# Kernel optimization log

Measured on AMD Instinct MI355X. Metric: run time of the kernel, lower is better.

Reference implementation:

```python
import jax, jax.numpy as jnp
import numpy as np

B, N, D, F = 32, 4096, 256, 256

def setup_inputs() -> dict:
    key = jax.random.key(0)
    k1, k2, k3, k4 = jax.random.split(key, 4)
    raw_input = jax.random.normal(k1, (B, N, D), dtype=jnp.float32)
    input_plus_attention = jax.random.normal(k2, (B, F), dtype=jnp.float32)
    W = jax.random.normal(k3, (F, N), dtype=jnp.float32) * 0.02
    b = jnp.zeros((N,), dtype=jnp.float32)
    # keras 'uniform' initializer: U(-0.05, 0.05)
    threshold = jax.random.uniform(k4, (1,), minval=-0.05, maxval=0.05, dtype=jnp.float32)
    return {"raw_input": raw_input, "input_plus_attention": input_plus_attention,
            "W": W, "b": b, "threshold": threshold}

def reference(raw_input, input_plus_attention, W, b, threshold):
    # Dense(units, relu): [B,F] @ [F,N] -> [B,N]
    x = jax.nn.relu(input_plus_attention @ W + b)
    # BinaryLayer: 1.0 where x > threshold else 0.0 -> row selection mask [B,N]
    mask = x > threshold[0]
    # TF boolean_mask + reshape(B,-1,D) performs per-batch stream compaction of
    # selected rows. JAX needs static shapes, so compact selected rows to the
    # front (stable order preserved) and zero-pad the tail to length N.
    order = jnp.argsort(jnp.where(mask, 0, 1).astype(jnp.int32), axis=1)  # stable: selected first
    gathered = jnp.take_along_axis(raw_input, order[:, :, None], axis=1)  # [B,N,D]
    counts = jnp.sum(mask, axis=1, keepdims=True)                          # [B,1]
    keep = jnp.arange(N)[None, :] < counts                                 # [B,N]
    out = jnp.where(keep[:, :, None], gathered, jnp.zeros((), raw_input.dtype))
    return out
```

## Files before the change

### kernel.cpp

```cpp
#include <hip/hip_runtime.h>
#include <hip/hip_bf16.h>
#include <stdint.h>


#define BB 32
#define NN 4096
#define DD 256
#define FF 256
#define ASTRIDE (FF + 4)
#define RPB 32

typedef float f4 __attribute__((ext_vector_type(4)));

__global__ __launch_bounds__(256) void mask_kernel(
    const float* __restrict__ A,
    const float* __restrict__ W,
    const float* __restrict__ bias,
    const float* __restrict__ thr_p,
    uint8_t* __restrict__ bits8)
{
    __shared__ float a_sh[BB * ASTRIDE];
    __shared__ float wT[8 * ASTRIDE];

    const int t     = threadIdx.x;
    const int chunk = blockIdx.x;
    const int n0    = chunk * 8;

    for (int i = t; i < BB * FF; i += 256) {
        int b = i >> 8, f = i & 255;
        a_sh[b * ASTRIDE + f] = A[i];
    }
    for (int i = t; i < FF * 8; i += 256) {
        int f = i >> 3, c = i & 7;
        wT[c * ASTRIDE + f] = W[(size_t)f * NN + n0 + c];
    }
    __syncthreads();

    const float thr = thr_p[0];
    const int c = t & 7;
    const int b = t >> 3;

    const f4* ap = reinterpret_cast<const f4*>(a_sh + b * ASTRIDE);
    const f4* wp = reinterpret_cast<const f4*>(wT   + c * ASTRIDE);

    double s0 = 0.0, s1 = 0.0, s2 = 0.0, s3 = 0.0;
    #pragma unroll 8
    for (int fs = 0; fs < FF / 4; ++fs) {
        f4 a4 = ap[fs];
        f4 w4 = wp[fs];
        s0 = fma((double)a4.x, (double)w4.x, s0);
        s1 = fma((double)a4.y, (double)w4.y, s1);
        s2 = fma((double)a4.z, (double)w4.z, s2);
        s3 = fma((double)a4.w, (double)w4.w, s3);
    }
    const float v = (float)((s0 + s1) + (s2 + s3)) + bias[n0 + c];
    const int m = (fmaxf(v, 0.f) > thr) ? 1 : 0;

    unsigned long long bal = __ballot(m);
    if (c == 0) {
        const int g = (t & 63) >> 3;
        bits8[b * 512 + chunk] = (uint8_t)((bal >> (8 * g)) & 0xFF);
    }
}

__global__ __launch_bounds__(256) void gather_kernel(
    const float* __restrict__ raw,
    const uint16_t* __restrict__ bits,
    float* __restrict__ out)
{
    const int b   = blockIdx.y;
    const int t   = threadIdx.x;
    const int j0b = blockIdx.x * RPB;

    __shared__ int wsum[4];
    __shared__ int cnt_sh;
    __shared__ int order_sh[RPB];

    unsigned m = bits[b * 256 + t];
    const int s = __popc(m);

    const int lane = t & 63;
    const int wid  = t >> 6;
    int incl = s;
    #pragma unroll
    for (int d = 1; d < 64; d <<= 1) {
        int x = __shfl_up(incl, d, 64);
        if (lane >= d) incl += x;
    }
    if (lane == 63) wsum[wid] = incl;
    __syncthreads();
    if (t == 0) {
        int run = 0;
        #pragma unroll
        for (int i = 0; i < 4; ++i) { int x = wsum[i]; wsum[i] = run; run += x; }
        cnt_sh = run;
    }
    __syncthreads();

    int base = wsum[wid] + (incl - s);
    if (base < j0b + RPB && base + s > j0b) {
        const int n0 = t * 16;
        while (m) {
            const int pos = __ffs(m) - 1;
            const unsigned rel = (unsigned)(base - j0b);
            if (rel < RPB) order_sh[rel] = n0 + pos;
            ++base;
            if (base >= j0b + RPB) break;
            m &= m - 1;
        }
    }
    __syncthreads();

    const int cnt = cnt_sh;
    const f4* rawb = reinterpret_cast<const f4*>(raw) + (size_t)b * NN * (DD / 4);
    f4*       outb = reinterpret_cast<f4*>(out)       + (size_t)b * NN * (DD / 4);
    const int j0 = j0b + wid * 8;

    #pragma unroll
    for (int g = 0; g < 2; ++g) {
        const int r = j0 + g * 4;
        const int rr = r - j0b;
        f4 v0 = {0.f, 0.f, 0.f, 0.f};
        f4 v1 = {0.f, 0.f, 0.f, 0.f};
        f4 v2 = {0.f, 0.f, 0.f, 0.f};
        f4 v3 = {0.f, 0.f, 0.f, 0.f};
        if (r + 0 < cnt) v0 = rawb[(size_t)order_sh[rr + 0] * (DD / 4) + lane];
        if (r + 1 < cnt) v1 = rawb[(size_t)order_sh[rr + 1] * (DD / 4) + lane];
        if (r + 2 < cnt) v2 = rawb[(size_t)order_sh[rr + 2] * (DD / 4) + lane];
        if (r + 3 < cnt) v3 = rawb[(size_t)order_sh[rr + 3] * (DD / 4) + lane];
        __builtin_nontemporal_store(v0, &outb[(size_t)(r + 0) * (DD / 4) + lane]);
        __builtin_nontemporal_store(v1, &outb[(size_t)(r + 1) * (DD / 4) + lane]);
        __builtin_nontemporal_store(v2, &outb[(size_t)(r + 2) * (DD / 4) + lane]);
        __builtin_nontemporal_store(v3, &outb[(size_t)(r + 3) * (DD / 4) + lane]);
    }
}

extern "C" void kernel_launch(void* const* d_in, const int* in_sizes, int n_in,
                              void* d_out, int out_size, void* d_ws, size_t ws_size,
                              hipStream_t stream) {
    const float* raw  = (const float*)d_in[0];
    const float* A    = (const float*)d_in[1];
    const float* W    = (const float*)d_in[2];
    const float* bias = (const float*)d_in[3];
    const float* thr  = (const float*)d_in[4];
    float* out = (float*)d_out;

    uint8_t* bits8 = (uint8_t*)d_ws;

    mask_kernel<<<512, 256, 0, stream>>>(A, W, bias, thr, bits8);
    gather_kernel<<<dim3(NN / RPB, BB), 256, 0, stream>>>(
        raw, (const uint16_t*)bits8, out);
}
```

Before: 55.85 us.

## Convert compaction gather into scatter with coalesced source loads and split zero-fill

Each block now loads its 32 contiguous source rows up front with non-temporal loads, overlapping them with the prefix scan. It computes destination indices per source row and scatters only the selected rows. Zero-padding of the tail is distributed evenly across blocks. This trades selective reads for full contiguous reads, increasing read traffic when few rows are selected, in exchange for early, coalesced loads and a simpler index build.

```diff
diff --git a/kernel.cpp b/kernel.cpp
--- a/kernel.cpp
+++ b/kernel.cpp
@@ -9,6 +9,7 @@
 #define FF 256
 #define ASTRIDE (FF + 4)
 #define RPB 32
+#define NBLK (NN / RPB)
 
 typedef float f4 __attribute__((ext_vector_type(4)));
 
@@ -68,19 +69,34 @@
     const uint16_t* __restrict__ bits,
     float* __restrict__ out)
 {
-    const int b   = blockIdx.y;
-    const int t   = threadIdx.x;
-    const int j0b = blockIdx.x * RPB;
+    const int b    = blockIdx.y;
+    const int bx   = blockIdx.x;
+    const int t    = threadIdx.x;
+    const int lane = t & 63;
+    const int wid  = t >> 6;
 
     __shared__ int wsum[4];
     __shared__ int cnt_sh;
-    __shared__ int order_sh[RPB];
+    __shared__ int dst_sh[RPB];
+
+    const f4* rawb = reinterpret_cast<const f4*>(raw) + (size_t)b * NN * (DD / 4);
+    f4*       outb = reinterpret_cast<f4*>(out)       + (size_t)b * NN * (DD / 4);
+    const int srow = bx * RPB + wid * 8;
+
+    f4 v0 = __builtin_nontemporal_load(&rawb[(size_t)(srow + 0) * (DD / 4) + lane]);
+    f4 v1 = __builtin_nontemporal_load(&rawb[(size_t)(srow + 1) * (DD / 4) + lane]);
+    f4 v2 = __builtin_nontemporal_load(&rawb[(size_t)(srow + 2) * (DD / 4) + lane]);
+    f4 v3 = __builtin_nontemporal_load(&rawb[(size_t)(srow + 3) * (DD / 4) + lane]);
+    f4 v4 = __builtin_nontemporal_load(&rawb[(size_t)(srow + 4) * (DD / 4) + lane]);
+    f4 v5 = __builtin_nontemporal_load(&rawb[(size_t)(srow + 5) * (DD / 4) + lane]);
+    f4 v6 = __builtin_nontemporal_load(&rawb[(size_t)(srow + 6) * (DD / 4) + lane]);
+    f4 v7 = __builtin_nontemporal_load(&rawb[(size_t)(srow + 7) * (DD / 4) + lane]);
+
+    if (t < RPB) dst_sh[t] = -1;
 
     unsigned m = bits[b * 256 + t];
     const int s = __popc(m);
 
-    const int lane = t & 63;
-    const int wid  = t >> 6;
     int incl = s;
     #pragma unroll
     for (int d = 1; d < 64; d <<= 1) {
@@ -97,42 +113,44 @@
     }
     __syncthreads();
 
-    int base = wsum[wid] + (incl - s);
-    if (base < j0b + RPB && base + s > j0b) {
-        const int n0 = t * 16;
-        while (m) {
-            const int pos = __ffs(m) - 1;
-            const unsigned rel = (unsigned)(base - j0b);
-            if (rel < RPB) order_sh[rel] = n0 + pos;
-            ++base;
-            if (base >= j0b + RPB) break;
-            m &= m - 1;
+    const int wchunk0 = bx * 2;
+    if (t == wchunk0 || t == wchunk0 + 1) {
+        const int loc0 = (t - wchunk0) * 16;
+        int d = wsum[wid] + (incl - s);
+        unsigned mm = m;
+        while (mm) {
+            const int pos = __ffs(mm) - 1;
+            dst_sh[loc0 + pos] = d++;
+            mm &= mm - 1;
         }
     }
     __syncthreads();
 
+    const int r0 = wid * 8;
+    const int d0 = dst_sh[r0 + 0];
+    const int d1 = dst_sh[r0 + 1];
+    const int d2 = dst_sh[r0 + 2];
+    const int d3 = dst_sh[r0 + 3];
+    const int d4 = dst_sh[r0 + 4];
+    const int d5 = dst_sh[r0 + 5];
+    const int d6 = dst_sh[r0 + 6];
+    const int d7 = dst_sh[r0 + 7];
+    if (d0 >= 0) __builtin_nontemporal_store(v0, &outb[(size_t)d0 * (DD / 4) + lane]);
+    if (d1 >= 0) __builtin_nontemporal_store(v1, &outb[(size_t)d1 * (DD / 4) + lane]);
+    if (d2 >= 0) __builtin_nontemporal_store(v2, &outb[(size_t)d2 * (DD / 4) + lane]);
+    if (d3 >= 0) __builtin_nontemporal_store(v3, &outb[(size_t)d3 * (DD / 4) + lane]);
+    if (d4 >= 0) __builtin_nontemporal_store(v4, &outb[(size_t)d4 * (DD / 4) + lane]);
+    if (d5 >= 0) __builtin_nontemporal_store(v5, &outb[(size_t)d5 * (DD / 4) + lane]);
+    if (d6 >= 0) __builtin_nontemporal_store(v6, &outb[(size_t)d6 * (DD / 4) + lane]);
+    if (d7 >= 0) __builtin_nontemporal_store(v7, &outb[(size_t)d7 * (DD / 4) + lane]);
+
     const int cnt = cnt_sh;
-    const f4* rawb = reinterpret_cast<const f4*>(raw) + (size_t)b * NN * (DD / 4);
-    f4*       outb = reinterpret_cast<f4*>(out)       + (size_t)b * NN * (DD / 4);
-    const int j0 = j0b + wid * 8;
-
-    #pragma unroll
-    for (int g = 0; g < 2; ++g) {
-        const int r = j0 + g * 4;
-        const int rr = r - j0b;
-        f4 v0 = {0.f, 0.f, 0.f, 0.f};
-        f4 v1 = {0.f, 0.f, 0.f, 0.f};
-        f4 v2 = {0.f, 0.f, 0.f, 0.f};
-        f4 v3 = {0.f, 0.f, 0.f, 0.f};
-        if (r + 0 < cnt) v0 = rawb[(size_t)order_sh[rr + 0] * (DD / 4) + lane];
-        if (r + 1 < cnt) v1 = rawb[(size_t)order_sh[rr + 1] * (DD / 4) + lane];
-        if (r + 2 < cnt) v2 = rawb[(size_t)order_sh[rr + 2] * (DD / 4) + lane];
-        if (r + 3 < cnt) v3 = rawb[(size_t)order_sh[rr + 3] * (DD / 4) + lane];
-        __builtin_nontemporal_store(v0, &outb[(size_t)(r + 0) * (DD / 4) + lane]);
-        __builtin_nontemporal_store(v1, &outb[(size_t)(r + 1) * (DD / 4) + lane]);
-        __builtin_nontemporal_store(v2, &outb[(size_t)(r + 2) * (DD / 4) + lane]);
-        __builtin_nontemporal_store(v3, &outb[(size_t)(r + 3) * (DD / 4) + lane]);
-    }
+    const int zn  = NN - cnt;
+    const int z0  = cnt + (int)(((long long)bx * zn) >> 7);
+    const int z1  = cnt + (int)(((long long)(bx + 1) * zn) >> 7);
+    const f4 zero = {0.f, 0.f, 0.f, 0.f};
+    for (int r = z0 + wid; r < z1; r += 4)
+        __builtin_nontemporal_store(zero, &outb[(size_t)r * (DD / 4) + lane]);
 }
 
 extern "C" void kernel_launch(void* const* d_in, const int* in_sizes, int n_in,
@@ -148,6 +166,6 @@
     uint8_t* bits8 = (uint8_t*)d_ws;
 
     mask_kernel<<<512, 256, 0, stream>>>(A, W, bias, thr, bits8);
-    gather_kernel<<<dim3(NN / RPB, BB), 256, 0, stream>>>(
+    gather_kernel<<<dim3(NBLK, BB), 256, 0, stream>>>(
         raw, (const uint16_t*)bits8, out);
 }
```

Measured after the change: 57.14 us. +2.3%, slower.
